# Performance work log

Hardware: AMD Instinct MI355X
Metric: run time of the kernel (lower is better)

## Reference

```python
import jax, jax.numpy as jnp
import numpy as np

N_NUM = 8
N_CAT = 4
CARD = 100
D_NUM = 16
D_CAT = 16
D_OUT = N_NUM * D_NUM + N_CAT * D_CAT  # 192
D_HID = 256
TEMP = 1.0


def setup_inputs() -> dict:
    key = jax.random.key(0)
    ks = jax.random.split(key, 12)
    B, N = 512, 131072
    x_num = jax.random.normal(ks[0], (B, N_NUM), dtype=jnp.float32)
    x_cat = jax.random.randint(ks[1], (B, N_CAT), 0, CARD)
    cand_x_num = jax.random.normal(ks[2], (N, N_NUM), dtype=jnp.float32)
    cand_x_cat = jax.random.randint(ks[3], (N, N_CAT), 0, CARD)
    cand_y = jax.random.uniform(ks[4], (N, 10), dtype=jnp.float32)
    s = 0.05
    W_num = jax.random.normal(ks[5], (N_NUM, D_NUM), dtype=jnp.float32) * s
    b_num = jax.random.normal(ks[6], (N_NUM, D_NUM), dtype=jnp.float32) * s
    emb = jax.random.normal(ks[7], (N_CAT, CARD, D_CAT), dtype=jnp.float32) * s
    W1 = jax.random.normal(ks[8], (D_OUT, D_HID), dtype=jnp.float32) * s
    b1 = jnp.zeros((D_HID,), dtype=jnp.float32)
    W2 = jax.random.normal(ks[9], (D_HID, D_OUT), dtype=jnp.float32) * s
    b2 = jnp.zeros((D_OUT,), dtype=jnp.float32)
    return dict(x_num=x_num, x_cat=x_cat, cand_x_num=cand_x_num,
                cand_x_cat=cand_x_cat, cand_y=cand_y, W_num=W_num, b_num=b_num,
                emb=emb, W1=W1, b1=b1, W2=W2, b2=b2)


def _encode(x_num, x_cat, W_num, b_num, emb):
    # per-numerical-feature linear embedding: [B, n_num, d_num]
    num_e = x_num[:, :, None] * W_num[None] + b_num[None]
    # categorical lookup: emb[f, x_cat[:, f]] -> [B, n_cat, d_cat]
    cat_e = emb[jnp.arange(N_CAT)[None, :], x_cat]
    B = x_num.shape[0]
    return jnp.concatenate([num_e.reshape(B, -1), cat_e.reshape(B, -1)], axis=-1)


def _block(z, W1, b1, W2, b2):
    # residual MLP block: d_out -> hidden -> d_out
    return z + jax.nn.relu(z @ W1 + b1) @ W2 + b2


def reference(x_num, x_cat, cand_x_num, cand_x_cat, cand_y,
              W_num, b_num, emb, W1, b1, W2, b2):
    x = _encode(x_num, x_cat, W_num, b_num, emb)            # [B, d]
    c = _encode(cand_x_num, cand_x_cat, W_num, b_num, emb)  # [N, d]
    x = _block(x, W1, b1, W2, b2)
    c = _block(c, W1, b1, W2, b2)
    d2 = (jnp.sum(x * x, axis=-1)[:, None] + jnp.sum(c * c, axis=-1)[None, :]
          - 2.0 * (x @ c.T))
    dist = jnp.sqrt(jnp.maximum(d2, 0.0)) / TEMP            # [B, N]
    probs = jax.nn.softmax(-dist, axis=-1)
    return probs @ cand_y                                    # [B, 10]
```

## Files before the change

### kernel.cpp

```cpp
#include <hip/hip_runtime.h>
#include <hip/hip_bf16.h>

typedef __bf16 bf16;
typedef __attribute__((ext_vector_type(8))) __bf16 bf16x8;
typedef __attribute__((ext_vector_type(4))) __bf16 bf16x4;
typedef __attribute__((ext_vector_type(4))) float f32x4;

#define NQ     512
#define NC     131072
#define DIM    192
#define HID    256
#define NY     10
#define NSLICE 512

#define KL2E   2.0813689810056077f
#define N2KL2E -4.1627379620112154f

#define OFF_W1B 0u
#define OFF_W2B (OFF_W1B + 49152u)
#define OFF_XE8 (OFF_W2B + 49152u)
#define OFF_X2  (OFF_XE8 + 98304u)
#define OFF_CE8 (OFF_X2 + 2048u)
#define OFF_C2  (OFF_CE8 + 25165824u)
#define OFF_P   (OFF_C2 + 524288u)
#define OFF_YB  (OFF_P + 12582912u)

static __device__ __forceinline__ unsigned pk4(float a, float b, float c, float d) {
  unsigned w = __builtin_amdgcn_cvt_pk_fp8_f32(a, b, 0, false);
  w = __builtin_amdgcn_cvt_pk_fp8_f32(c, d, w, true);
  return w;
}

__global__ __launch_bounds__(256) void k_prep(const float* __restrict__ W1,
                                              const float* __restrict__ W2,
                                              const float* __restrict__ cy,
                                              unsigned char* __restrict__ W1B8,
                                              unsigned char* __restrict__ W2B8,
                                              bf16* __restrict__ YB) {
  if (blockIdx.x < 384) {
    int idx = blockIdx.x * 256 + threadIdx.x;
    if (idx < 192 * 256) {
      int k = idx / 256, n = idx % 256;
      int p = (k >> 5) * 4 + ((k >> 3) & 3);
      int pk = __builtin_amdgcn_cvt_pk_fp8_f32(W1[idx], W1[idx], 0, false);
      W1B8[((size_t)(p * 256 + n)) * 8 + (k & 7)] = (unsigned char)(pk & 0xff);
    } else {
      int i2 = idx - 192 * 256;
      int k = i2 / 192, n = i2 % 192;
      int p = (k >> 5) * 4 + ((k >> 3) & 3);
      int pk = __builtin_amdgcn_cvt_pk_fp8_f32(W2[i2], W2[i2], 0, false);
      W2B8[((size_t)(p * 192 + n)) * 8 + (k & 7)] = (unsigned char)(pk & 0xff);
    }
  } else {
    int u = (blockIdx.x - 384) * 256 + threadIdx.x;
    int p32 = u >> 6, lane6 = u & 63;
    int qq = lane6 >> 4, l15 = lane6 & 15;
    bf16x8 v;
#pragma unroll
    for (int jj = 0; jj < 8; jj++) {
      int cand = p32 * 32 + qq * 8 + jj;
      float x = (l15 < 10) ? cy[(size_t)cand * NY + l15] : (l15 == 10 ? 1.f : 0.f);
      v[jj] = (bf16)x;
    }
    *(bf16x8*)&YB[(size_t)u * 8] = v;
  }
}

__global__ __launch_bounds__(256, 4) void k_encode(
    const float* __restrict__ xnq, const int* __restrict__ xcq,
    const float* __restrict__ xnc, const int* __restrict__ xcc,
    const float* __restrict__ Wn, const float* __restrict__ bn,
    const float* __restrict__ emb, const float* __restrict__ b1,
    const float* __restrict__ b2, const unsigned char* __restrict__ W1B8,
    const unsigned char* __restrict__ W2B8, unsigned char* __restrict__ ce8,
    unsigned char* __restrict__ xe8, float* __restrict__ x2v,
    float* __restrict__ c2v) {
  __shared__ alignas(16) unsigned char zt8[64][208];
  __shared__ alignas(16) unsigned char hth8[64][264];
  __shared__ float n2l[64];

  const int t = threadIdx.x;
  const bool isq = blockIdx.x < 8;
  const int row0 = (isq ? blockIdx.x : blockIdx.x - 8) * 64;
  const float* __restrict__ xn = isq ? xnq : xnc;
  const int* __restrict__ xc = isq ? xcq : xcc;
  const int lane = t & 63, w = t >> 6;
  const int l15 = lane & 15, q = lane >> 4;

  if (t < 64) n2l[t] = 0.f;

  {
    const int g = row0 + lane;
    float2 xv2 = *(const float2*)&xn[(size_t)g * 8 + 2 * w];
    int cv = xc[g * 4 + w];
#pragma unroll
    for (int f01 = 0; f01 < 2; f01++) {
      int f = 2 * w + f01;
      float xv = f01 ? xv2.y : xv2.x;
      float zz[16];
#pragma unroll
      for (int i = 0; i < 4; i++) {
        f32x4 wv = *(const f32x4*)&Wn[f * 16 + i * 4];
        f32x4 bv = *(const f32x4*)&bn[f * 16 + i * 4];
#pragma unroll
        for (int u = 0; u < 4; u++) zz[i * 4 + u] = xv * wv[u] + bv[u];
      }
      uint4 pk;
      pk.x = pk4(zz[0], zz[1], zz[2], zz[3]);
      pk.y = pk4(zz[4], zz[5], zz[6], zz[7]);
      pk.z = pk4(zz[8], zz[9], zz[10], zz[11]);
      pk.w = pk4(zz[12], zz[13], zz[14], zz[15]);
      *(uint4*)&zt8[lane][f * 16] = pk;
    }
    const float* er = &emb[(size_t)(w * 100 + cv) * 16];
    f32x4 e0 = *(const f32x4*)&er[0];
    f32x4 e1 = *(const f32x4*)&er[4];
    f32x4 e2 = *(const f32x4*)&er[8];
    f32x4 e3 = *(const f32x4*)&er[12];
    uint4 pk;
    pk.x = pk4(e0[0], e0[1], e0[2], e0[3]);
    pk.y = pk4(e1[0], e1[1], e1[2], e1[3]);
    pk.z = pk4(e2[0], e2[1], e2[2], e2[3]);
    pk.w = pk4(e3[0], e3[1], e3[2], e3[3]);
    *(uint4*)&zt8[lane][128 + w * 16] = pk;
  }
  __syncthreads();

  f32x4 z4 = {0.f, 0.f, 0.f, 0.f};

  {
    f32x4 acc1[4][4];
#pragma unroll
    for (int mi = 0; mi < 4; mi++)
#pragma unroll
      for (int ni = 0; ni < 4; ni++) acc1[mi][ni] = z4;
#pragma unroll 2
    for (int kk = 0; kk < 192; kk += 32) {
      long a[4], b[4];
#pragma unroll
      for (int mi = 0; mi < 4; mi++)
        a[mi] = *(const long*)&zt8[mi * 16 + l15][kk + q * 8];
      const unsigned char* wp = &W1B8[(size_t)(((kk >> 5) * 4 + q) * 256 + w * 64 + l15) * 8];
#pragma unroll
      for (int ni = 0; ni < 4; ni++)
        b[ni] = *(const long*)&wp[ni * 128];
#pragma unroll
      for (int mi = 0; mi < 4; mi++)
#pragma unroll
        for (int ni = 0; ni < 4; ni++)
          acc1[mi][ni] = __builtin_amdgcn_mfma_f32_16x16x32_fp8_fp8(b[ni], a[mi], acc1[mi][ni], 0, 0, 0);
    }
#pragma unroll
    for (int ni = 0; ni < 4; ni++) {
      f32x4 bb = *(const f32x4*)&b1[w * 64 + ni * 16 + q * 4];
#pragma unroll
      for (int mi = 0; mi < 4; mi++) {
        float h0 = acc1[mi][ni][0] + bb[0]; h0 = h0 > 0.f ? h0 : 0.f;
        float h1 = acc1[mi][ni][1] + bb[1]; h1 = h1 > 0.f ? h1 : 0.f;
        float h2 = acc1[mi][ni][2] + bb[2]; h2 = h2 > 0.f ? h2 : 0.f;
        float h3 = acc1[mi][ni][3] + bb[3]; h3 = h3 > 0.f ? h3 : 0.f;
        *(unsigned*)&hth8[mi * 16 + l15][w * 64 + ni * 16 + q * 4] = pk4(h0, h1, h2, h3);
      }
    }
  }
  __syncthreads();

  f32x4 acc2[4][3];
#pragma unroll
  for (int mi = 0; mi < 4; mi++)
#pragma unroll
    for (int ni = 0; ni < 3; ni++) acc2[mi][ni] = z4;
#pragma unroll 2
  for (int kk = 0; kk < 256; kk += 32) {
    long a[4], b[3];
#pragma unroll
    for (int mi = 0; mi < 4; mi++)
      a[mi] = *(const long*)&hth8[mi * 16 + l15][kk + q * 8];
    const unsigned char* wp = &W2B8[(size_t)(((kk >> 5) * 4 + q) * 192 + w * 48 + l15) * 8];
#pragma unroll
    for (int ni = 0; ni < 3; ni++)
      b[ni] = *(const long*)&wp[ni * 128];
#pragma unroll
    for (int mi = 0; mi < 4; mi++)
#pragma unroll
      for (int ni = 0; ni < 3; ni++)
        acc2[mi][ni] = __builtin_amdgcn_mfma_f32_16x16x32_fp8_fp8(b[ni], a[mi], acc2[mi][ni], 0, 0, 0);
  }

  {
    float nrm[4];
#pragma unroll
    for (int mi = 0; mi < 4; mi++) nrm[mi] = 0.f;
#pragma unroll
    for (int ni = 0; ni < 3; ni++) {
      const int n0 = w * 48 + ni * 16 + q * 4;
      f32x4 bb = *(const f32x4*)&b2[n0];
#pragma unroll
      for (int mi = 0; mi < 4; mi++) {
        const int rr = mi * 16 + l15;
        unsigned old = *(const unsigned*)&zt8[rr][n0];
        float v0 = __builtin_amdgcn_cvt_f32_fp8((int)old, 0) + acc2[mi][ni][0] + bb[0];
        float v1 = __builtin_amdgcn_cvt_f32_fp8((int)old, 1) + acc2[mi][ni][1] + bb[1];
        float v2 = __builtin_amdgcn_cvt_f32_fp8((int)old, 2) + acc2[mi][ni][2] + bb[2];
        float v3 = __builtin_amdgcn_cvt_f32_fp8((int)old, 3) + acc2[mi][ni][3] + bb[3];
        unsigned pkw = pk4(v0, v1, v2, v3);
        *(unsigned*)&zt8[rr][n0] = pkw;
        float r0 = __builtin_amdgcn_cvt_f32_fp8((int)pkw, 0);
        float r1 = __builtin_amdgcn_cvt_f32_fp8((int)pkw, 1);
        float r2 = __builtin_amdgcn_cvt_f32_fp8((int)pkw, 2);
        float r3 = __builtin_amdgcn_cvt_f32_fp8((int)pkw, 3);
        nrm[mi] += r0 * r0 + r1 * r1 + r2 * r2 + r3 * r3;
      }
    }
#pragma unroll
    for (int mi = 0; mi < 4; mi++) {
      float s = nrm[mi];
      s += __shfl_xor(s, 16);
      s += __shfl_xor(s, 32);
      if (lane < 16) atomicAdd(&n2l[mi * 16 + l15], s);
    }
  }
  __syncthreads();

  if (isq) {
    for (int cc = w; cc < 24; cc += 4) {
      long v = *(const long*)&zt8[lane][cc * 8];
      *(long*)&xe8[((size_t)cc * NQ + row0 + lane) * 8] = v;
    }
    if (t < 64) x2v[row0 + t] = n2l[t] * KL2E;
  } else {
    for (int cc = w; cc < 24; cc += 4) {
      long v = *(const long*)&zt8[lane][cc * 8];
      *(long*)&ce8[((size_t)cc * NC + row0 + lane) * 8] = v;
    }
    if (t < 64) c2v[row0 + t] = n2l[t] * KL2E;
  }
}

__global__ __launch_bounds__(256, 4) void k_dist(
    const unsigned char* __restrict__ xe8, const float* __restrict__ x2v,
    const unsigned char* __restrict__ ce8, const float* __restrict__ c2v,
    const bf16* __restrict__ YB, float* __restrict__ P) {
  __shared__ alignas(16) bf16 ET[4][16][40];
  __shared__ alignas(16) float Pst[256 * 12];

  const int t = threadIdx.x;
  const int raw = blockIdx.x;
  const int half = raw >> 9;
  const int r9 = raw & (NSLICE - 1);
  const int slice = (r9 & 7) * 64 + (r9 >> 3);
  const int n0 = slice * 256;
  const int qh = half * 256;
  const int lane = t & 63, w = t >> 6;
  const int l15 = lane & 15, q = lane >> 4;
  const int qbase = qh + w * 64;

  f32x4 z4 = {0.f, 0.f, 0.f, 0.f};
  f32x4 oacc[4];
#pragma unroll
  for (int nq = 0; nq < 4; nq++) oacc[nq] = z4;

  float x2a[4];
#pragma unroll
  for (int nq = 0; nq < 4; nq++) x2a[nq] = x2v[qbase + nq * 16 + l15];

#pragma unroll 1
  for (int c = 0; c < 4; ++c) {
#pragma unroll
    for (int mch = 0; mch < 2; mch++) {
      f32x4 acc[2][4];
#pragma unroll
      for (int mc2 = 0; mc2 < 2; mc2++)
#pragma unroll
        for (int nq = 0; nq < 4; nq++) acc[mc2][nq] = z4;

#pragma unroll
      for (int ks = 0; ks < 6; ks++) {
        long a[2], b[4];
        const unsigned char* cp =
            &ce8[((size_t)(ks * 4 + q) * NC + n0 + c * 64 + mch * 32 + l15) * 8];
#pragma unroll
        for (int mc2 = 0; mc2 < 2; mc2++)
          a[mc2] = *(const long*)&cp[mc2 * 128];
        const unsigned char* xp =
            &xe8[(size_t)((ks * 4 + q) * NQ + qbase + l15) * 8];
#pragma unroll
        for (int nq = 0; nq < 4; nq++)
          b[nq] = *(const long*)&xp[nq * 128];
#pragma unroll
        for (int mc2 = 0; mc2 < 2; mc2++)
#pragma unroll
          for (int nq = 0; nq < 4; nq++)
            acc[mc2][nq] = __builtin_amdgcn_mfma_f32_16x16x32_fp8_fp8(a[mc2], b[nq], acc[mc2][nq], 0, 0, 0);
      }

      bf16x8 yf = *(const bf16x8*)&YB[((size_t)(slice * 8 + c * 2 + mch) * 64 + lane) * 8];
      f32x4 c2p[2];
#pragma unroll
      for (int mc2 = 0; mc2 < 2; mc2++)
        c2p[mc2] = *(const f32x4*)&c2v[n0 + c * 64 + mch * 32 + mc2 * 16 + q * 4];

#pragma unroll
      for (int nq = 0; nq < 4; ++nq) {
#pragma unroll
        for (int mc2 = 0; mc2 < 2; mc2++) {
          bf16x4 ev;
#pragma unroll
          for (int r = 0; r < 4; r++) {
            float d2 = __builtin_fmaf(N2KL2E, acc[mc2][nq][r], x2a[nq] + c2p[mc2][r]);
            ev[r] = (bf16)__builtin_amdgcn_exp2f(-__builtin_amdgcn_sqrtf(__builtin_fabsf(d2)));
          }
          *(bf16x4*)&ET[w][l15][mc2 * 16 + q * 4] = ev;
        }
        bf16x8 a = *(const bf16x8*)&ET[w][l15][q * 8];
        oacc[nq] = __builtin_amdgcn_mfma_f32_16x16x32_bf16(a, yf, oacc[nq], 0, 0, 0);
      }
    }
  }

  if (l15 < 11) {
#pragma unroll
    for (int nq = 0; nq < 4; nq++)
#pragma unroll
      for (int r = 0; r < 4; r++) {
        int lq = w * 64 + nq * 16 + q * 4 + r;
        Pst[lq * 12 + l15] = oacc[nq][r];
      }
  }
  __syncthreads();
  {
    const f32x4* Ps = (const f32x4*)Pst;
    float* Pb = P + ((size_t)qh * NSLICE + slice) * 12;
#pragma unroll
    for (int i = t; i < 768; i += 256) {
      int lq = i / 3, part = i % 3;
      *(f32x4*)&Pb[(size_t)lq * NSLICE * 12 + part * 4] = Ps[i];
    }
  }
}

__global__ __launch_bounds__(512) void k_comb(const float* __restrict__ P,
                                              float* __restrict__ out) {
  __shared__ float red[8][11];
  const int t = threadIdx.x;
  const int qy = blockIdx.x;
  const int lane = t & 63, w = t >> 6;

  const float* p = &P[((size_t)qy * NSLICE + t) * 12];
  f32x4 v0 = *(const f32x4*)&p[0];
  f32x4 v1 = *(const f32x4*)&p[4];
  f32x4 v2 = *(const f32x4*)&p[8];
  float s[11];
#pragma unroll
  for (int j = 0; j < 4; j++) s[j] = v0[j];
#pragma unroll
  for (int j = 0; j < 4; j++) s[4 + j] = v1[j];
#pragma unroll
  for (int j = 0; j < 3; j++) s[8 + j] = v2[j];
#pragma unroll
  for (int d = 1; d < 64; d <<= 1)
#pragma unroll
    for (int j = 0; j < 11; j++) s[j] += __shfl_xor(s[j], d);
  if (lane == 0)
#pragma unroll
    for (int j = 0; j < 11; j++) red[w][j] = s[j];
  __syncthreads();
  if (t < 10) {
    float o = 0.f, l = 0.f;
#pragma unroll
    for (int i = 0; i < 8; i++) { o += red[i][t]; l += red[i][10]; }
    out[qy * NY + t] = o / l;
  }
}

extern "C" void kernel_launch(void* const* d_in, const int* in_sizes, int n_in,
                              void* d_out, int out_size, void* d_ws, size_t ws_size,
                              hipStream_t stream) {
  (void)in_sizes; (void)n_in; (void)out_size; (void)ws_size;
  const float* x_num = (const float*)d_in[0];
  const int*   x_cat = (const int*)d_in[1];
  const float* c_num = (const float*)d_in[2];
  const int*   c_cat = (const int*)d_in[3];
  const float* c_y   = (const float*)d_in[4];
  const float* W_num = (const float*)d_in[5];
  const float* b_num = (const float*)d_in[6];
  const float* emb   = (const float*)d_in[7];
  const float* W1    = (const float*)d_in[8];
  const float* b1    = (const float*)d_in[9];
  const float* W2    = (const float*)d_in[10];
  const float* b2    = (const float*)d_in[11];
  float* out = (float*)d_out;

  char* ws = (char*)d_ws;
  unsigned char* W1B8 = (unsigned char*)(ws + OFF_W1B);
  unsigned char* W2B8 = (unsigned char*)(ws + OFF_W2B);
  unsigned char* xe8  = (unsigned char*)(ws + OFF_XE8);
  float* x2v = (float*)(ws + OFF_X2);
  unsigned char* ce8  = (unsigned char*)(ws + OFF_CE8);
  float* c2v = (float*)(ws + OFF_C2);
  float* P   = (float*)(ws + OFF_P);
  bf16*  YB  = (bf16*)(ws + OFF_YB);

  k_prep<<<dim3(1408), dim3(256), 0, stream>>>(W1, W2, c_y, W1B8, W2B8, YB);
  k_encode<<<dim3(8 + NC / 64), dim3(256), 0, stream>>>(
      x_num, x_cat, c_num, c_cat, W_num, b_num, emb, b1, b2, W1B8, W2B8,
      ce8, xe8, x2v, c2v);
  k_dist<<<dim3(2 * NSLICE), dim3(256), 0, stream>>>(xe8, x2v, ce8, c2v, YB, P);
  k_comb<<<dim3(NQ), dim3(512), 0, stream>>>(P, out);
}
```

Measured before the change: 178.4 us.

## Store candidate fp8 rows contiguously and stage tiles through double-buffered LDS

The encoder now writes candidate fp8 embeddings row-major (192 bytes per row) instead of the 8-byte-chunk column-interleaved layout. The distance kernel loads each 64-candidate tile with coalesced 16-byte loads into a double-buffered, padded LDS buffer, prefetching the next tile into registers while the MFMAs run on the current one. The aim is to replace many scattered 8-byte global loads with wide coalesced loads and to overlap them with compute. This costs extra LDS (reused for the output staging), a barrier per tile, and more register pressure.

```diff
diff --git a/kernel.cpp b/kernel.cpp
--- a/kernel.cpp
+++ b/kernel.cpp
@@ -229,9 +229,12 @@
     }
     if (t < 64) x2v[row0 + t] = n2l[t] * KL2E;
   } else {
-    for (int cc = w; cc < 24; cc += 4) {
-      long v = *(const long*)&zt8[lane][cc * 8];
-      *(long*)&ce8[((size_t)cc * NC + row0 + lane) * 8] = v;
+    unsigned int* dst = (unsigned int*)(ce8 + (size_t)row0 * DIM);
+#pragma unroll
+    for (int i = 0; i < 12; i++) {
+      int j = t + 256 * i;
+      int r = j / 48, cb = (j - r * 48) * 4;
+      dst[j] = *(const unsigned int*)&zt8[r][cb];
     }
     if (t < 64) c2v[row0 + t] = n2l[t] * KL2E;
   }
@@ -241,8 +244,8 @@
     const unsigned char* __restrict__ xe8, const float* __restrict__ x2v,
     const unsigned char* __restrict__ ce8, const float* __restrict__ c2v,
     const bf16* __restrict__ YB, float* __restrict__ P) {
+  __shared__ alignas(16) unsigned char ct8[2][64][208];
   __shared__ alignas(16) bf16 ET[4][16][40];
-  __shared__ alignas(16) float Pst[256 * 12];
 
   const int t = threadIdx.x;
   const int raw = blockIdx.x;
@@ -254,6 +257,7 @@
   const int lane = t & 63, w = t >> 6;
   const int l15 = lane & 15, q = lane >> 4;
   const int qbase = qh + w * 64;
+  const int sr = t >> 2, squ = t & 3;
 
   f32x4 z4 = {0.f, 0.f, 0.f, 0.f};
   f32x4 oacc[4];
@@ -264,8 +268,23 @@
 #pragma unroll
   for (int nq = 0; nq < 4; nq++) x2a[nq] = x2v[qbase + nq * 16 + l15];
 
+  {
+    const uint4* src = (const uint4*)(ce8 + (size_t)(n0 + sr) * DIM + squ * 48);
+    uint4* dst = (uint4*)&ct8[0][sr][squ * 48];
+#pragma unroll
+    for (int i = 0; i < 3; i++) dst[i] = src[i];
+  }
+
 #pragma unroll 1
   for (int c = 0; c < 4; ++c) {
+    const int cb = c & 1;
+    uint4 pf0, pf1, pf2;
+    if (c < 3) {
+      const uint4* src = (const uint4*)(ce8 + (size_t)(n0 + (c + 1) * 64 + sr) * DIM + squ * 48);
+      pf0 = src[0]; pf1 = src[1]; pf2 = src[2];
+    }
+    __syncthreads();
+
 #pragma unroll
     for (int mch = 0; mch < 2; mch++) {
       f32x4 acc[2][4];
@@ -274,16 +293,13 @@
 #pragma unroll
         for (int nq = 0; nq < 4; nq++) acc[mc2][nq] = z4;
 
-#pragma unroll
-      for (int ks = 0; ks < 6; ks++) {
+#pragma unroll 2
+      for (int kk = 0; kk < 192; kk += 32) {
         long a[2], b[4];
-        const unsigned char* cp =
-            &ce8[((size_t)(ks * 4 + q) * NC + n0 + c * 64 + mch * 32 + l15) * 8];
 #pragma unroll
         for (int mc2 = 0; mc2 < 2; mc2++)
-          a[mc2] = *(const long*)&cp[mc2 * 128];
-        const unsigned char* xp =
-            &xe8[(size_t)((ks * 4 + q) * NQ + qbase + l15) * 8];
+          a[mc2] = *(const long*)&ct8[cb][(mch * 2 + mc2) * 16 + l15][kk + q * 8];
+        const unsigned char* xp = &xe8[(size_t)(((kk >> 5) * 4 + q) * NQ + qbase + l15) * 8];
 #pragma unroll
         for (int nq = 0; nq < 4; nq++)
           b[nq] = *(const long*)&xp[nq * 128];
@@ -316,8 +332,15 @@
         oacc[nq] = __builtin_amdgcn_mfma_f32_16x16x32_bf16(a, yf, oacc[nq], 0, 0, 0);
       }
     }
-  }
-
+
+    if (c < 3) {
+      uint4* dst = (uint4*)&ct8[cb ^ 1][sr][squ * 48];
+      dst[0] = pf0; dst[1] = pf1; dst[2] = pf2;
+    }
+  }
+
+  __syncthreads();
+  float* Pst = (float*)&ct8[0][0][0];
   if (l15 < 11) {
 #pragma unroll
     for (int nq = 0; nq < 4; nq++)
```

Measured after the change: 156.3 us. 12.4% less time.
